# Performance work log

Measured on AMD Instinct MI355X. Metric: run time of the kernel, lower is better.

Reference implementation:

```python
import jax, jax.numpy as jnp
import numpy as np

B, A, NB = 8, 1024, 64          # batch, atoms, neighbors
NAB, NF, NG, NI = 128, 128, 25, 3  # atom basis, filters, gaussians, interactions
CUT = 5.0
MAXZ = 100
LOG2 = float(np.log(2.0))

def ssp(x):
    # shifted softplus: log(0.5) + softplus(x)
    return jax.nn.softplus(x) - LOG2

def setup_inputs() -> dict:
    key = jax.random.key(0)
    ks = jax.random.split(key, 12)
    positions = jax.random.uniform(ks[0], (B, A, 3), jnp.float32, 0.0, 10.0)
    cell = jnp.zeros((B, 3, 3), jnp.float32)
    cell_offset = jnp.zeros((B, A, NB, 3), jnp.float32)
    # self-avoiding neighbor indices in [0, A)
    off = jax.random.randint(ks[1], (B, A, NB), 1, A)
    neighbors = ((jnp.arange(A)[None, :, None] + off) % A).astype(jnp.int32)
    neighbor_mask = jnp.ones((B, A, NB), jnp.float32)
    atom_mask = jnp.ones((B, A), jnp.float32)
    atomic_numbers = jax.random.randint(ks[2], (B, A), 1, MAXZ).astype(jnp.int32)
    s = 0.05
    emb = (jax.random.normal(ks[3], (MAXZ, NAB)) * 0.1).at[0].set(0.0)  # padding_idx=0
    fw1 = jax.random.normal(ks[4], (NI, NG, NF)) * s
    fb1 = jnp.zeros((NI, NF), jnp.float32)
    fw2 = jax.random.normal(ks[5], (NI, NF, NF)) * s
    fb2 = jnp.zeros((NI, NF), jnp.float32)
    in2f_w = jax.random.normal(ks[6], (NI, NAB, NF)) * s
    f2out_w = jax.random.normal(ks[7], (NI, NF, NAB)) * s
    f2out_b = jnp.zeros((NI, NAB), jnp.float32)
    dense_w = jax.random.normal(ks[8], (NI, NAB, NAB)) * s
    dense_b = jnp.zeros((NI, NAB), jnp.float32)
    return dict(positions=positions, cell=cell, cell_offset=cell_offset,
                neighbor_mask=neighbor_mask, atom_mask=atom_mask,
                emb=emb, fw1=fw1, fb1=fb1, fw2=fw2, fb2=fb2,
                in2f_w=in2f_w, f2out_w=f2out_w, f2out_b=f2out_b,
                dense_w=dense_w, dense_b=dense_b,
                atomic_numbers=atomic_numbers, neighbors=neighbors)

def reference(positions, cell, cell_offset, neighbor_mask, atom_mask,
              emb, fw1, fb1, fw2, fb2, in2f_w, f2out_w, f2out_b,
              dense_w, dense_b, atomic_numbers, neighbors):
    x = emb[atomic_numbers]                                   # (B,A,NAB)
    nb = neighbors.reshape(B, A * NB)
    # atom distances with PBC offsets
    pos_j = jnp.take_along_axis(positions, nb[..., None], axis=1).reshape(B, A, NB, 3)
    pos_j = pos_j + jnp.einsum('banc,bcd->band', cell_offset, cell)
    dvec = pos_j - positions[:, :, None, :]
    d2 = jnp.sum(dvec * dvec, axis=-1)                        # (B,A,NB)
    r_ij = jnp.sqrt(jnp.where(neighbor_mask > 0, d2, 1.0)) * neighbor_mask
    # gaussian smearing of distances
    offsets = jnp.linspace(0.0, CUT, NG, dtype=jnp.float32)
    width = offsets[1] - offsets[0]
    coeff = -0.5 / (width * width)
    f_ij = jnp.exp(coeff * (r_ij[..., None] - offsets) ** 2)  # (B,A,NB,NG)
    # cosine cutoff
    C = 0.5 * (jnp.cos(r_ij * jnp.pi / CUT) + 1.0) * (r_ij < CUT)
    for i in range(NI):
        # filter-generating network
        W = ssp(f_ij @ fw1[i] + fb1[i]) @ fw2[i] + fb2[i]     # (B,A,NB,NF)
        W = W * C[..., None]
        # CFConv: project, gather neighbors, modulate, scatter-sum
        y = x @ in2f_w[i]                                     # (B,A,NF)
        y_nbh = jnp.take_along_axis(y, nb[..., None], axis=1).reshape(B, A, NB, NF)
        agg = jnp.sum(y_nbh * W * neighbor_mask[..., None], axis=2)  # (B,A,NF)
        v = ssp(agg @ f2out_w[i] + f2out_b[i])                # (B,A,NAB)
        v = v @ dense_w[i] + dense_b[i]
        x = x + v
    return x
```

## Files before the change

### kernel.cpp

```cpp
#include <hip/hip_runtime.h>

typedef __attribute__((ext_vector_type(8))) short bf16x8;
typedef __attribute__((ext_vector_type(4))) float f32x4;
typedef __attribute__((ext_vector_type(2))) unsigned int u32x2;
typedef __attribute__((ext_vector_type(4))) unsigned int u32x4;
typedef __attribute__((ext_vector_type(2))) __bf16 bf16x2t;
typedef unsigned short u16;
typedef unsigned int u32;
typedef unsigned long long u64;

#define DI __device__ __forceinline__

#define NKNOT 2048

DI float b2f(u16 u){ union{u32 i; float f;} v; v.i = ((u32)u)<<16; return v.f; }
DI float asf(u32 u){ union{u32 i; float f;} v; v.i = u; return v.f; }
DI u16 f2b(float f){ union{float f; u32 i;} v; v.f=f; u32 u=v.i;
                     return (u16)((u + 0x7fffu + ((u>>16)&1u))>>16); }
DI u32 pk2(float lo, float hi){
#if __has_builtin(__builtin_amdgcn_cvt_pk_bf16_f32)
  bf16x2t h = __builtin_amdgcn_cvt_pk_bf16_f32(lo, hi);
  u32 d; __builtin_memcpy(&d, &h, 4); return d;
#else
  return (u32)f2b(lo) | ((u32)f2b(hi)<<16);
#endif
}
DI float fexp2(float x){
#if __has_builtin(__builtin_amdgcn_exp2f)
  return __builtin_amdgcn_exp2f(x);
#else
  return __expf(x*0.6931471805599453f);
#endif
}
DI float flog2(float x){
#if __has_builtin(__builtin_amdgcn_logf)
  return __builtin_amdgcn_logf(x);
#else
  return __logf(x)*1.4426950408889634f;
#endif
}
DI float ldin(const void* p, size_t i, int isbf){
  return isbf ? b2f(((const u16*)p)[i]) : ((const float*)p)[i];
}
DI f32x4 ldin4(const void* p, size_t i, int isbf){
  if(isbf){
    u32x2 d = *(const u32x2*)((const u16*)p + i);
    f32x4 r;
    r[0] = b2f((u16)(d[0]&0xffff)); r[1] = b2f((u16)(d[0]>>16));
    r[2] = b2f((u16)(d[1]&0xffff)); r[3] = b2f((u16)(d[1]>>16));
    return r;
  }
  return *(const f32x4*)((const float*)p + i);
}
DI int probe_bf(const void* nmask){ return ((const u16*)nmask)[0] == 0x3F80u; }

DI f32x4 mfma16(bf16x8 a, bf16x8 b, f32x4 c){
  return __builtin_amdgcn_mfma_f32_16x16x32_bf16(a,b,c,0,0,0);
}
DI bf16x8 ldfragA_f32(const float* p){
  f32x4 a = ((const f32x4*)p)[0], b = ((const f32x4*)p)[1];
  union{ u32 d[4]; bf16x8 v; } u;
  u.d[0]=pk2(a[0],a[1]); u.d[1]=pk2(a[2],a[3]);
  u.d[2]=pk2(b[0],b[1]); u.d[3]=pk2(b[2],b[3]);
  return u.v;
}
DI float sspf(float x){ return __logf(1.f + __expf(x)) - 0.6931471805599453f; }

#define WF_STRIDE 73728
#define WF_FW2    4096
#define WF_IN2F   24576
#define WF_F2O    40960
#define WF_DEN    57344

__global__ __launch_bounds__(256) void k_setup(const void* __restrict__ pos,
                                               const void* __restrict__ cell,
                                               const void* __restrict__ cello,
                                               const void* __restrict__ nmask,
                                               const void* __restrict__ emb,
                                               const void* __restrict__ fw1,
                                               const void* __restrict__ fb1,
                                               const void* __restrict__ fw2,
                                               const void* __restrict__ fb2,
                                               const void* __restrict__ in2f,
                                               const void* __restrict__ f2o,
                                               const void* __restrict__ den,
                                               const int* __restrict__ z,
                                               const int* __restrict__ nbrs,
                                               float* __restrict__ X,
                                               u32x2* __restrict__ DESC,
                                               u32* __restrict__ CNT,
                                               u16* __restrict__ WF){
  int isbf = probe_bf(nmask);
  int bx = blockIdx.x, tid = threadIdx.x;
  if(bx < 1024){
    int idx = bx*256 + tid;
    int a = idx>>5, f4 = (idx&31)*4;
    f32x4 e = ldin4(emb, (size_t)z[a]*128 + f4, isbf);
    *(f32x4*)(X + (size_t)a*128 + f4) = e;
    return;
  }
  if(bx < 3072){
    int pairIdx = (bx-1024)*256 + tid;
    int atom = pairIdx>>6;
    int lane = tid & 63;
    int b = atom>>10;
    int nb = nbrs[pairIdx];
    int jrow = (b<<10) + nb;
    float pi0=ldin(pos,atom*3+0,isbf), pi1=ldin(pos,atom*3+1,isbf), pi2=ldin(pos,atom*3+2,isbf);
    float pj0=ldin(pos,jrow*3+0,isbf), pj1=ldin(pos,jrow*3+1,isbf), pj2=ldin(pos,jrow*3+2,isbf);
    float co0=ldin(cello,(size_t)pairIdx*3+0,isbf),
          co1=ldin(cello,(size_t)pairIdx*3+1,isbf),
          co2=ldin(cello,(size_t)pairIdx*3+2,isbf);
    size_t cb = (size_t)b*9;
    pj0 += co0*ldin(cell,cb+0,isbf) + co1*ldin(cell,cb+3,isbf) + co2*ldin(cell,cb+6,isbf);
    pj1 += co0*ldin(cell,cb+1,isbf) + co1*ldin(cell,cb+4,isbf) + co2*ldin(cell,cb+7,isbf);
    pj2 += co0*ldin(cell,cb+2,isbf) + co1*ldin(cell,cb+5,isbf) + co2*ldin(cell,cb+8,isbf);
    float d0 = pj0-pi0, d1 = pj1-pi1, d2 = pj2-pi2;
    float dd = d0*d0 + d1*d1 + d2*d2;
    float m  = ldin(nmask,pairIdx,isbf);
    float r  = sqrtf(m>0.f ? dd : 1.f) * m;
    float c  = 0.5f*(__cosf(r*3.14159265358979f/5.f)+1.f) * ((r<5.f)?1.f:0.f) * m;
    float s  = r * ((float)(NKNOT-1)/5.0f);
    int   k  = (int)s; if(k > NKNOT-2) k = NKNOT-2;
    float fr = s - (float)k;
    float a0 = c*(1.f-fr), a1 = c*fr;
    union{ _Float16 h[2]; u32 u; } pa;
    pa.h[0] = (_Float16)a0; pa.h[1] = (_Float16)a1;
    int act = (c > 0.f);
    u64 bal = __ballot(act);
    u64 below = bal & ((1ULL<<lane)-1ULL);
    int cnt = (int)__popcll(bal);
    int apre = (int)__popcll(below);
    int pos_ = act ? apre : (cnt + (lane - apre));
    u32x2 dsc;
    if(act){ dsc[0] = pa.u; dsc[1] = (u32)k | ((u32)nb<<16); }
    else   { dsc[0] = 0u;   dsc[1] = 0u; }
    DESC[(size_t)atom*64 + pos_] = dsc;
    if(lane == 0) CNT[atom] = (u32)cnt;
    return;
  }
  int wid = (bx-3072)*4 + (tid>>6);
  int lane = tid & 63;
  int q = lane>>4, l15 = lane&15;
  int i = wid/144, r = wid%144;
  int mat, kk, t;
  if(r < 8){ mat=0; kk=0; t=r; }
  else if(r < 48){ int r2 = r-8; mat=1; kk=r2>>3; t=r2&7; }
  else { int r3 = r-48; mat = 2 + (r3>>5); kk = (r3>>3)&3; t = r3&7; }
  const void* src; size_t sbase; int K; int off;
  switch(mat){
    case 0:  src = fw1;  sbase=(size_t)i*3200;  K=25;  off=0;       break;
    case 1:  src = fw2;  sbase=(size_t)i*16384; K=128; off=WF_FW2;  break;
    case 2:  src = in2f; sbase=(size_t)i*16384; K=128; off=WF_IN2F; break;
    case 3:  src = f2o;  sbase=(size_t)i*16384; K=128; off=WF_F2O;  break;
    default: src = den;  sbase=(size_t)i*16384; K=128; off=WF_DEN;  break;
  }
  int c = t*16 + l15;
  bf16x8 frag;
  #pragma unroll
  for(int j=0;j<8;j++){
    int k = kk*32 + q*8 + j;
    float v;
    if(k < K)                 v = ldin(src, sbase + (size_t)k*128 + c, isbf);
    else if(mat==0 && k==25)  v = ldin(fb1, (size_t)i*128 + c, isbf);
    else if(mat==1 && k==128) v = ldin(fb2, (size_t)i*128 + c, isbf);
    else                      v = 0.f;
    if(mat==0) v *= 1.4426950408889634f;
    frag[j] = (short)f2b(v);
  }
  *(bf16x8*)(WF + (size_t)i*WF_STRIDE + off + ((kk*8+t)*64 + lane)*8) = frag;
}

__global__ __launch_bounds__(256) void k_mid(const u16* __restrict__ WF,
                                             u32x2* __restrict__ TT,
                                             const float* __restrict__ X,
                                             float* __restrict__ Y){
  __shared__ __align__(16) u16 Hb[4][16][168];
  int tid = threadIdx.x;
  int widx = tid>>6;
  int lane = tid & 63;
  int q = lane>>4, l15 = lane&15;
  int bx = blockIdx.x;

  if(bx >= 96){
    int wid2 = (bx-96)*4 + widx;
    int row0 = wid2*16;
    const u16* wf = WF + WF_IN2F;
    f32x4 acc[8];
    #pragma unroll
    for(int t=0;t<8;t++) acc[t] = (f32x4){0.f,0.f,0.f,0.f};
    #pragma unroll
    for(int kk=0;kk<4;kk++){
      bf16x8 xf = ldfragA_f32(X + (size_t)(row0+l15)*128 + kk*32 + q*8);
      #pragma unroll
      for(int t=0;t<8;t++){
        bf16x8 wv = *(const bf16x8*)(wf + ((kk*8+t)*64 + lane)*8);
        acc[t] = mfma16(wv, xf, acc[t]);
      }
    }
    #pragma unroll
    for(int t=0;t<8;t++)
      *(f32x4*)(Y + (size_t)(row0+l15)*128 + t*16 + q*4) = acc[t];
    return;
  }

  int wid = bx*4 + widx;
  int i  = wid>>7;
  int kb = (wid&127)*16;
  const u16* fw1f = WF + (size_t)i*WF_STRIDE;
  const u16* fw2f = WF + (size_t)i*WF_STRIDE + WF_FW2;
  u16 (*H)[168] = Hb[widx];

  const float width = 5.0f/24.0f;
  const float c2 = (-0.5f/(width*width))*1.4426950408889634f;
  float r = (float)(kb + l15) * (5.0f/(float)(NKNOT-1));

  float gv[8];
  #pragma unroll
  for(int j=0;j<8;j++){
    int k = q*8+j;
    if(k < 25){ float t = fmaf(-width,(float)k,r); gv[j] = fexp2(c2*t*t); }
    else gv[j] = (k==25) ? 1.f : 0.f;
  }
  union{ u32 d[4]; bf16x8 v; } afu;
  afu.d[0]=pk2(gv[0],gv[1]); afu.d[1]=pk2(gv[2],gv[3]);
  afu.d[2]=pk2(gv[4],gv[5]); afu.d[3]=pk2(gv[6],gv[7]);
  bf16x8 af = afu.v;

  f32x4 acc[8];
  #pragma unroll
  for(int t=0;t<8;t++){
    bf16x8 w1 = *(const bf16x8*)(fw1f + (size_t)t*512 + lane*8);
    acc[t] = mfma16(w1, af, (f32x4){0.f,0.f,0.f,0.f});
  }
  const float ln2 = 0.69314718055994531f;
  #pragma unroll
  for(int t=0;t<8;t++){
    float h0 = fmaf(flog2(1.f+fexp2(acc[t][0])), ln2, -ln2);
    float h1 = fmaf(flog2(1.f+fexp2(acc[t][1])), ln2, -ln2);
    float h2 = fmaf(flog2(1.f+fexp2(acc[t][2])), ln2, -ln2);
    float h3 = fmaf(flog2(1.f+fexp2(acc[t][3])), ln2, -ln2);
    u32x2 d; d[0]=pk2(h0,h1); d[1]=pk2(h2,h3);
    *(u32x2*)(&H[l15][t*16 + q*4]) = d;
  }
  {
    u32x2 zb; zb[0] = (q==0) ? pk2(1.f, 0.f) : 0u; zb[1] = 0u;
    *(u32x2*)(&H[l15][128 + q*4]) = zb;
    u32x2 zz; zz[0]=0u; zz[1]=0u;
    *(u32x2*)(&H[l15][144 + q*4]) = zz;
  }
  #pragma unroll
  for(int t=0;t<8;t++) acc[t] = (f32x4){0.f,0.f,0.f,0.f};
  #pragma unroll
  for(int kk=0;kk<5;kk++){
    bf16x8 a2 = *(const bf16x8*)(&H[l15][kk*32 + q*8]);
    #pragma unroll
    for(int t=0;t<8;t++){
      bf16x8 wv = *(const bf16x8*)(fw2f + ((kk*8+t)*64 + lane)*8);
      acc[t] = mfma16(a2, wv, acc[t]);
    }
  }
  {
    u32x2* ttb = TT + (size_t)i*NKNOT*64;
    int row = kb + l15;
    #pragma unroll
    for(int t=0;t<8;t++){
      u32 d0 = pk2(acc[t][0],acc[t][1]);
      u32 d1 = pk2(acc[t][2],acc[t][3]);
      int l = t*8 + q*2;
      ((u32*)&ttb[(size_t)row*64 + l    ])[0] = d0;
      ((u32*)&ttb[(size_t)row*64 + l + 1])[0] = d1;
      if(row > 0){
        ((u32*)&ttb[(size_t)(row-1)*64 + l    ])[1] = d0;
        ((u32*)&ttb[(size_t)(row-1)*64 + l + 1])[1] = d1;
      }
    }
  }
}

__global__ __launch_bounds__(512, 8) void k_iter(const u32x2* __restrict__ desc,
                                                 const u32* __restrict__ CNT,
                                                 const u32x2* __restrict__ TT,
                                                 const float* __restrict__ Yr,
                                                 float* __restrict__ X,
                                                 float* __restrict__ Yw,
                                                 const u16* __restrict__ f2of,
                                                 const u16* __restrict__ denf,
                                                 const u16* __restrict__ in2fN,
                                                 const void* __restrict__ f2ob,
                                                 const void* __restrict__ denb,
                                                 const void* __restrict__ nmask,
                                                 void* __restrict__ OUT,
                                                 int last, int iidx){
  __shared__ __align__(16) float AGGs[16][132];
  __shared__ __align__(16) u16 Tb[16][136];
  __shared__ __align__(16) u16 Xw[16][136];
  int isbf = probe_bf(nmask);
  int widx = threadIdx.x>>6;
  int lane = threadIdx.x & 63;
  int q = lane>>4, l15 = lane&15;
  int bid = blockIdx.x;
  int row0 = (bid & 7)*1024 + (bid >> 3)*8;

  {
    int atom = row0 + widx;
    int cnt = (int)__builtin_amdgcn_readfirstlane(CNT[atom]);
    int ng  = (cnt + 3) >> 2;
    u32x2 dsc = desc[(size_t)atom*64 + lane];
    const char* Yb = (const char*)(Yr + (size_t)(atom & ~1023)*128);
    const char* Tc = (const char*)TT;
    int h   = lane>>5;
    int j32 = lane&31;
    int boff = j32<<4;
    f32x4 acc4 = (f32x4){0.f,0.f,0.f,0.f};
    #pragma unroll 1
    for(int g=0; g<ng; ++g){
      u32 cu[2]; u32x4 tt[2]; f32x4 yv[2];
      #pragma unroll
      for(int s=0; s<2; ++s){
        int p0 = g*4 + s*2;
        u32 d1a = __builtin_amdgcn_readlane(dsc[1], p0);
        u32 d1b = __builtin_amdgcn_readlane(dsc[1], p0+1);
        u32 d0a = __builtin_amdgcn_readlane(dsc[0], p0);
        u32 d0b = __builtin_amdgcn_readlane(dsc[0], p0+1);
        u32 d1 = h ? d1b : d1a;
        cu[s]  = h ? d0b : d0a;
        u32 krow = d1 & 0xffffu;
        u32 nbr  = d1 >> 16;
        tt[s] = *(const u32x4*)(Tc + ((size_t)krow<<9) + boff);
        yv[s] = *(const f32x4*)(Yb + ((size_t)nbr<<9) + boff);
      }
      #pragma unroll
      for(int s=0; s<2; ++s){
        union{ u32 u; _Float16 hh[2]; } pa; pa.u = cu[s];
        float a0 = (float)pa.hh[0], a1 = (float)pa.hh[1];
        float w0 = fmaf(a1, asf(tt[s][1]<<16),          a0*asf(tt[s][0]<<16));
        float w1 = fmaf(a1, asf(tt[s][1]&0xffff0000u),  a0*asf(tt[s][0]&0xffff0000u));
        float w2 = fmaf(a1, asf(tt[s][3]<<16),          a0*asf(tt[s][2]<<16));
        float w3 = fmaf(a1, asf(tt[s][3]&0xffff0000u),  a0*asf(tt[s][2]&0xffff0000u));
        acc4[0] = fmaf(w0, yv[s][0], acc4[0]);
        acc4[1] = fmaf(w1, yv[s][1], acc4[1]);
        acc4[2] = fmaf(w2, yv[s][2], acc4[2]);
        acc4[3] = fmaf(w3, yv[s][3], acc4[3]);
      }
    }
    *(f32x4*)(&AGGs[widx + 8*h][j32*4]) = acc4;
  }
  __syncthreads();

  {
    int t = widx;
    f32x4 acc = (f32x4){0.f,0.f,0.f,0.f};
    #pragma unroll
    for(int kk=0;kk<4;kk++){
      bf16x8 gf = ldfragA_f32(&AGGs[l15][kk*32 + q*8]);
      bf16x8 wv = *(const bf16x8*)(f2of + ((kk*8+t)*64 + lane)*8);
      acc = mfma16(wv, gf, acc);
    }
    #pragma unroll
    for(int r=0;r<4;r++) acc[r] += __shfl_xor(acc[r], 8);
    f32x4 bv = ldin4(f2ob, (size_t)iidx*128 + t*16 + q*4, isbf);
    u32x2 d;
    d[0] = pk2(sspf(acc[0]+bv[0]), sspf(acc[1]+bv[1]));
    d[1] = pk2(sspf(acc[2]+bv[2]), sspf(acc[3]+bv[3]));
    *(u32x2*)(&Tb[l15][t*16 + q*4]) = d;
  }
  __syncthreads();

  {
    int t = widx;
    f32x4 acc = (f32x4){0.f,0.f,0.f,0.f};
    #pragma unroll
    for(int kk=0;kk<4;kk++){
      bf16x8 tf = *(const bf16x8*)(&Tb[l15][kk*32 + q*8]);
      bf16x8 wv = *(const bf16x8*)(denf + ((kk*8+t)*64 + lane)*8);
      acc = mfma16(wv, tf, acc);
    }
    size_t idx = (size_t)(row0+l15)*128 + t*16 + q*4;
    f32x4 bv = ldin4(denb, (size_t)iidx*128 + t*16 + q*4, isbf);
    f32x4 xv = *(const f32x4*)(X + idx);
    f32x4 xn;
    #pragma unroll
    for(int r=0;r<4;r++) xn[r] = xv[r] + acc[r] + bv[r];
    if(l15 < 8){
      *(f32x4*)(X + idx) = xn;
      if(last){
        if(isbf){
          u32x2 o; o[0]=pk2(xn[0],xn[1]); o[1]=pk2(xn[2],xn[3]);
          *(u32x2*)((u16*)OUT + idx) = o;
        } else {
          *(f32x4*)((float*)OUT + idx) = xn;
        }
      }
    }
    if(!last){
      u32x2 d; d[0]=pk2(xn[0],xn[1]); d[1]=pk2(xn[2],xn[3]);
      *(u32x2*)(&Xw[l15][t*16 + q*4]) = d;
    }
  }
  if(!last){
    __syncthreads();
    {
      int t = widx;
      f32x4 acc = (f32x4){0.f,0.f,0.f,0.f};
      #pragma unroll
      for(int kk=0;kk<4;kk++){
        bf16x8 xf = *(const bf16x8*)(&Xw[l15][kk*32 + q*8]);
        bf16x8 wv = *(const bf16x8*)(in2fN + ((kk*8+t)*64 + lane)*8);
        acc = mfma16(wv, xf, acc);
      }
      if(l15 < 8)
        *(f32x4*)(Yw + (size_t)(row0+l15)*128 + t*16 + q*4) = acc;
    }
  }
}

extern "C" void kernel_launch(void* const* d_in, const int* in_sizes, int n_in,
                              void* d_out, int out_size, void* d_ws, size_t ws_size,
                              hipStream_t stream){
  const void* pos   = d_in[0];
  const void* cell  = d_in[1];
  const void* cello = d_in[2];
  const void* nmask = d_in[3];
  const void* emb   = d_in[5];
  const void* fw1   = d_in[6];
  const void* fb1   = d_in[7];
  const void* fw2   = d_in[8];
  const void* fb2   = d_in[9];
  const void* in2f  = d_in[10];
  const void* f2o   = d_in[11];
  const void* f2ob  = d_in[12];
  const void* den   = d_in[13];
  const void* denb  = d_in[14];
  const int* z      = (const int*)d_in[15];
  const int* nbrs   = (const int*)d_in[16];

  char* ws = (char*)d_ws;
  float* X    = (float*)(ws);
  float* Y    = (float*)(ws +  4194304);
  float* Y2   = (float*)(ws +  8388608);
  u32x2* DESC = (u32x2*)(ws + 12582912);
  u16*   WF   = (u16*)  (ws + 16777216);
  u32x2* TT   = (u32x2*)(ws + 17301504);
  u32*   CNT  = (u32*)  (ws + 20447232);

  k_setup<<<3180, 256, 0, stream>>>(pos, cell, cello, nmask, emb,
                                    fw1, fb1, fw2, fb2, in2f, f2o, den,
                                    z, nbrs, X, DESC, CNT, WF);
  k_mid  <<< 224, 256, 0, stream>>>(WF, TT, X, Y);

  for(int i=0;i<3;i++){
    const u16* base = WF + (size_t)i*WF_STRIDE;
    const u16* in2fN = (i<2) ? (WF + (size_t)(i+1)*WF_STRIDE + WF_IN2F) : WF;
    const float* Yrd = (i&1) ? Y2 : Y;
    float*       Ywr = (i&1) ? Y  : Y2;
    k_iter<<<1024, 512, 0, stream>>>(DESC, CNT, TT + (size_t)i*NKNOT*64, Yrd, X, Ywr,
                                     base + WF_F2O, base + WF_DEN, in2fN,
                                     f2ob, denb, nmask,
                                     d_out, (i==2) ? 1 : 0, i);
  }
}
```

Before: 161.8 us.

## Merge setup and mid kernels into one launch reading raw weights directly

Combines the setup and mid kernels into a single launch. The filter-table and first-layer projection blocks now read fw1/fw2/in2f and the embedding straight from the inputs, converting to bf16 in registers, so they no longer depend on the pre-packed weight buffer or X written by other blocks. The aim is to remove one kernel launch and the serialization between the two stages. In exchange, those blocks do redundant strided global loads and conversions of the weights, and shared memory is now allocated for every block of the merged kernel.

```diff
diff --git a/kernel.cpp b/kernel.cpp
--- a/kernel.cpp
+++ b/kernel.cpp
@@ -67,31 +67,37 @@
 DI float sspf(float x){ return __logf(1.f + __expf(x)) - 0.6931471805599453f; }
 
 #define WF_STRIDE 73728
-#define WF_FW2    4096
 #define WF_IN2F   24576
 #define WF_F2O    40960
 #define WF_DEN    57344
 
-__global__ __launch_bounds__(256) void k_setup(const void* __restrict__ pos,
-                                               const void* __restrict__ cell,
-                                               const void* __restrict__ cello,
-                                               const void* __restrict__ nmask,
-                                               const void* __restrict__ emb,
-                                               const void* __restrict__ fw1,
-                                               const void* __restrict__ fb1,
-                                               const void* __restrict__ fw2,
-                                               const void* __restrict__ fb2,
-                                               const void* __restrict__ in2f,
-                                               const void* __restrict__ f2o,
-                                               const void* __restrict__ den,
-                                               const int* __restrict__ z,
-                                               const int* __restrict__ nbrs,
-                                               float* __restrict__ X,
-                                               u32x2* __restrict__ DESC,
-                                               u32* __restrict__ CNT,
-                                               u16* __restrict__ WF){
+__global__ __launch_bounds__(256) void k_all(const void* __restrict__ pos,
+                                             const void* __restrict__ cell,
+                                             const void* __restrict__ cello,
+                                             const void* __restrict__ nmask,
+                                             const void* __restrict__ emb,
+                                             const void* __restrict__ fw1,
+                                             const void* __restrict__ fb1,
+                                             const void* __restrict__ fw2,
+                                             const void* __restrict__ fb2,
+                                             const void* __restrict__ in2f,
+                                             const void* __restrict__ f2o,
+                                             const void* __restrict__ den,
+                                             const int* __restrict__ z,
+                                             const int* __restrict__ nbrs,
+                                             float* __restrict__ X,
+                                             u32x2* __restrict__ DESC,
+                                             u32* __restrict__ CNT,
+                                             u16* __restrict__ WF,
+                                             u32x2* __restrict__ TT,
+                                             float* __restrict__ Y){
+  __shared__ __align__(16) u16 Hb[4][16][168];
   int isbf = probe_bf(nmask);
   int bx = blockIdx.x, tid = threadIdx.x;
+  int widx = tid>>6;
+  int lane = tid & 63;
+  int q = lane>>4, l15 = lane&15;
+
   if(bx < 1024){
     int idx = bx*256 + tid;
     int a = idx>>5, f4 = (idx&31)*4;
@@ -102,7 +108,6 @@
   if(bx < 3072){
     int pairIdx = (bx-1024)*256 + tid;
     int atom = pairIdx>>6;
-    int lane = tid & 63;
     int b = atom>>10;
     int nb = nbrs[pairIdx];
     int jrow = (b<<10) + nb;
@@ -139,142 +144,150 @@
     if(lane == 0) CNT[atom] = (u32)cnt;
     return;
   }
-  int wid = (bx-3072)*4 + (tid>>6);
-  int lane = tid & 63;
-  int q = lane>>4, l15 = lane&15;
-  int i = wid/144, r = wid%144;
-  int mat, kk, t;
-  if(r < 8){ mat=0; kk=0; t=r; }
-  else if(r < 48){ int r2 = r-8; mat=1; kk=r2>>3; t=r2&7; }
-  else { int r3 = r-48; mat = 2 + (r3>>5); kk = (r3>>3)&3; t = r3&7; }
-  const void* src; size_t sbase; int K; int off;
-  switch(mat){
-    case 0:  src = fw1;  sbase=(size_t)i*3200;  K=25;  off=0;       break;
-    case 1:  src = fw2;  sbase=(size_t)i*16384; K=128; off=WF_FW2;  break;
-    case 2:  src = in2f; sbase=(size_t)i*16384; K=128; off=WF_IN2F; break;
-    case 3:  src = f2o;  sbase=(size_t)i*16384; K=128; off=WF_F2O;  break;
-    default: src = den;  sbase=(size_t)i*16384; K=128; off=WF_DEN;  break;
-  }
-  int c = t*16 + l15;
-  bf16x8 frag;
-  #pragma unroll
-  for(int j=0;j<8;j++){
-    int k = kk*32 + q*8 + j;
-    float v;
-    if(k < K)                 v = ldin(src, sbase + (size_t)k*128 + c, isbf);
-    else if(mat==0 && k==25)  v = ldin(fb1, (size_t)i*128 + c, isbf);
-    else if(mat==1 && k==128) v = ldin(fb2, (size_t)i*128 + c, isbf);
-    else                      v = 0.f;
-    if(mat==0) v *= 1.4426950408889634f;
-    frag[j] = (short)f2b(v);
-  }
-  *(bf16x8*)(WF + (size_t)i*WF_STRIDE + off + ((kk*8+t)*64 + lane)*8) = frag;
-}
-
-__global__ __launch_bounds__(256) void k_mid(const u16* __restrict__ WF,
-                                             u32x2* __restrict__ TT,
-                                             const float* __restrict__ X,
-                                             float* __restrict__ Y){
-  __shared__ __align__(16) u16 Hb[4][16][168];
-  int tid = threadIdx.x;
-  int widx = tid>>6;
-  int lane = tid & 63;
-  int q = lane>>4, l15 = lane&15;
-  int bx = blockIdx.x;
-
-  if(bx >= 96){
-    int wid2 = (bx-96)*4 + widx;
+  if(bx < 3144){
+    int wid = (bx-3072)*4 + widx;
+    int i = wid/96, r = wid%96;
+    int mat = r>>5, kk = (r>>3)&3, t = r&7;
+    const void* src; int off;
+    switch(mat){
+      case 0:  src = in2f; off=WF_IN2F; break;
+      case 1:  src = f2o;  off=WF_F2O;  break;
+      default: src = den;  off=WF_DEN;  break;
+    }
+    size_t sbase = (size_t)i*16384;
+    int c = t*16 + l15;
+    bf16x8 frag;
+    #pragma unroll
+    for(int j=0;j<8;j++){
+      int k = kk*32 + q*8 + j;
+      frag[j] = (short)f2b(ldin(src, sbase + (size_t)k*128 + c, isbf));
+    }
+    *(bf16x8*)(WF + (size_t)i*WF_STRIDE + off + ((kk*8+t)*64 + lane)*8) = frag;
+    return;
+  }
+  if(bx < 3240){
+    int wid = (bx-3144)*4 + widx;
+    int i  = wid>>7;
+    int kb = (wid&127)*16;
+    u16 (*H)[168] = Hb[widx];
+
+    const float width = 5.0f/24.0f;
+    const float c2 = (-0.5f/(width*width))*1.4426950408889634f;
+    const float l2e = 1.4426950408889634f;
+    float r = (float)(kb + l15) * (5.0f/(float)(NKNOT-1));
+
+    float gv[8];
+    #pragma unroll
+    for(int j=0;j<8;j++){
+      int k = q*8+j;
+      if(k < 25){ float t = fmaf(-width,(float)k,r); gv[j] = fexp2(c2*t*t); }
+      else gv[j] = (k==25) ? 1.f : 0.f;
+    }
+    union{ u32 d[4]; bf16x8 v; } afu;
+    afu.d[0]=pk2(gv[0],gv[1]); afu.d[1]=pk2(gv[2],gv[3]);
+    afu.d[2]=pk2(gv[4],gv[5]); afu.d[3]=pk2(gv[6],gv[7]);
+    bf16x8 af = afu.v;
+
+    f32x4 acc[8];
+    #pragma unroll
+    for(int t=0;t<8;t++){
+      int c = t*16 + l15;
+      union{ u32 d[4]; bf16x8 v; } wu;
+      #pragma unroll
+      for(int jj=0;jj<4;jj++){
+        int k0 = q*8 + jj*2, k1 = k0+1;
+        float v0 = (k0<25) ? ldin(fw1,(size_t)i*3200+(size_t)k0*128+c,isbf)
+                 : (k0==25 ? ldin(fb1,(size_t)i*128+c,isbf) : 0.f);
+        float v1 = (k1<25) ? ldin(fw1,(size_t)i*3200+(size_t)k1*128+c,isbf)
+                 : (k1==25 ? ldin(fb1,(size_t)i*128+c,isbf) : 0.f);
+        wu.d[jj] = pk2(v0*l2e, v1*l2e);
+      }
+      acc[t] = mfma16(wu.v, af, (f32x4){0.f,0.f,0.f,0.f});
+    }
+    const float ln2 = 0.69314718055994531f;
+    #pragma unroll
+    for(int t=0;t<8;t++){
+      float h0 = fmaf(flog2(1.f+fexp2(acc[t][0])), ln2, -ln2);
+      float h1 = fmaf(flog2(1.f+fexp2(acc[t][1])), ln2, -ln2);
+      float h2 = fmaf(flog2(1.f+fexp2(acc[t][2])), ln2, -ln2);
+      float h3 = fmaf(flog2(1.f+fexp2(acc[t][3])), ln2, -ln2);
+      u32x2 d; d[0]=pk2(h0,h1); d[1]=pk2(h2,h3);
+      *(u32x2*)(&H[l15][t*16 + q*4]) = d;
+    }
+    {
+      u32x2 zb; zb[0] = (q==0) ? pk2(1.f, 0.f) : 0u; zb[1] = 0u;
+      *(u32x2*)(&H[l15][128 + q*4]) = zb;
+      u32x2 zz; zz[0]=0u; zz[1]=0u;
+      *(u32x2*)(&H[l15][144 + q*4]) = zz;
+    }
+    #pragma unroll
+    for(int t=0;t<8;t++) acc[t] = (f32x4){0.f,0.f,0.f,0.f};
+    #pragma unroll
+    for(int kk=0;kk<5;kk++){
+      bf16x8 a2 = *(const bf16x8*)(&H[l15][kk*32 + q*8]);
+      #pragma unroll
+      for(int t=0;t<8;t++){
+        int c = t*16 + l15;
+        union{ u32 d[4]; bf16x8 v; } wu;
+        #pragma unroll
+        for(int jj=0;jj<4;jj++){
+          int k0 = kk*32 + q*8 + jj*2, k1 = k0+1;
+          float v0 = (k0<128) ? ldin(fw2,(size_t)i*16384+(size_t)k0*128+c,isbf)
+                   : (k0==128 ? ldin(fb2,(size_t)i*128+c,isbf) : 0.f);
+          float v1 = (k1<128) ? ldin(fw2,(size_t)i*16384+(size_t)k1*128+c,isbf)
+                   : (k1==128 ? ldin(fb2,(size_t)i*128+c,isbf) : 0.f);
+          wu.d[jj] = pk2(v0, v1);
+        }
+        acc[t] = mfma16(a2, wu.v, acc[t]);
+      }
+    }
+    {
+      u32x2* ttb = TT + (size_t)i*NKNOT*64;
+      int row = kb + l15;
+      #pragma unroll
+      for(int t=0;t<8;t++){
+        u32 d0 = pk2(acc[t][0],acc[t][1]);
+        u32 d1 = pk2(acc[t][2],acc[t][3]);
+        int l = t*8 + q*2;
+        ((u32*)&ttb[(size_t)row*64 + l    ])[0] = d0;
+        ((u32*)&ttb[(size_t)row*64 + l + 1])[0] = d1;
+        if(row > 0){
+          ((u32*)&ttb[(size_t)(row-1)*64 + l    ])[1] = d0;
+          ((u32*)&ttb[(size_t)(row-1)*64 + l + 1])[1] = d1;
+        }
+      }
+    }
+    return;
+  }
+  {
+    int wid2 = (bx-3240)*4 + widx;
     int row0 = wid2*16;
-    const u16* wf = WF + WF_IN2F;
+    int zr = z[row0 + l15];
     f32x4 acc[8];
     #pragma unroll
     for(int t=0;t<8;t++) acc[t] = (f32x4){0.f,0.f,0.f,0.f};
     #pragma unroll
     for(int kk=0;kk<4;kk++){
-      bf16x8 xf = ldfragA_f32(X + (size_t)(row0+l15)*128 + kk*32 + q*8);
+      bf16x8 xf;
+      if(isbf) xf = *(const bf16x8*)((const u16*)emb + (size_t)zr*128 + kk*32 + q*8);
+      else     xf = ldfragA_f32((const float*)emb + (size_t)zr*128 + kk*32 + q*8);
       #pragma unroll
       for(int t=0;t<8;t++){
-        bf16x8 wv = *(const bf16x8*)(wf + ((kk*8+t)*64 + lane)*8);
-        acc[t] = mfma16(wv, xf, acc[t]);
+        int c = t*16 + l15;
+        union{ u32 d[4]; bf16x8 v; } wu;
+        #pragma unroll
+        for(int jj=0;jj<4;jj++){
+          int k0 = kk*32 + q*8 + jj*2;
+          float v0 = ldin(in2f, (size_t)k0*128 + c, isbf);
+          float v1 = ldin(in2f, (size_t)(k0+1)*128 + c, isbf);
+          wu.d[jj] = pk2(v0, v1);
+        }
+        acc[t] = mfma16(wu.v, xf, acc[t]);
       }
     }
     #pragma unroll
     for(int t=0;t<8;t++)
       *(f32x4*)(Y + (size_t)(row0+l15)*128 + t*16 + q*4) = acc[t];
-    return;
-  }
-
-  int wid = bx*4 + widx;
-  int i  = wid>>7;
-  int kb = (wid&127)*16;
-  const u16* fw1f = WF + (size_t)i*WF_STRIDE;
-  const u16* fw2f = WF + (size_t)i*WF_STRIDE + WF_FW2;
-  u16 (*H)[168] = Hb[widx];
-
-  const float width = 5.0f/24.0f;
-  const float c2 = (-0.5f/(width*width))*1.4426950408889634f;
-  float r = (float)(kb + l15) * (5.0f/(float)(NKNOT-1));
-
-  float gv[8];
-  #pragma unroll
-  for(int j=0;j<8;j++){
-    int k = q*8+j;
-    if(k < 25){ float t = fmaf(-width,(float)k,r); gv[j] = fexp2(c2*t*t); }
-    else gv[j] = (k==25) ? 1.f : 0.f;
-  }
-  union{ u32 d[4]; bf16x8 v; } afu;
-  afu.d[0]=pk2(gv[0],gv[1]); afu.d[1]=pk2(gv[2],gv[3]);
-  afu.d[2]=pk2(gv[4],gv[5]); afu.d[3]=pk2(gv[6],gv[7]);
-  bf16x8 af = afu.v;
-
-  f32x4 acc[8];
-  #pragma unroll
-  for(int t=0;t<8;t++){
-    bf16x8 w1 = *(const bf16x8*)(fw1f + (size_t)t*512 + lane*8);
-    acc[t] = mfma16(w1, af, (f32x4){0.f,0.f,0.f,0.f});
-  }
-  const float ln2 = 0.69314718055994531f;
-  #pragma unroll
-  for(int t=0;t<8;t++){
-    float h0 = fmaf(flog2(1.f+fexp2(acc[t][0])), ln2, -ln2);
-    float h1 = fmaf(flog2(1.f+fexp2(acc[t][1])), ln2, -ln2);
-    float h2 = fmaf(flog2(1.f+fexp2(acc[t][2])), ln2, -ln2);
-    float h3 = fmaf(flog2(1.f+fexp2(acc[t][3])), ln2, -ln2);
-    u32x2 d; d[0]=pk2(h0,h1); d[1]=pk2(h2,h3);
-    *(u32x2*)(&H[l15][t*16 + q*4]) = d;
-  }
-  {
-    u32x2 zb; zb[0] = (q==0) ? pk2(1.f, 0.f) : 0u; zb[1] = 0u;
-    *(u32x2*)(&H[l15][128 + q*4]) = zb;
-    u32x2 zz; zz[0]=0u; zz[1]=0u;
-    *(u32x2*)(&H[l15][144 + q*4]) = zz;
-  }
-  #pragma unroll
-  for(int t=0;t<8;t++) acc[t] = (f32x4){0.f,0.f,0.f,0.f};
-  #pragma unroll
-  for(int kk=0;kk<5;kk++){
-    bf16x8 a2 = *(const bf16x8*)(&H[l15][kk*32 + q*8]);
-    #pragma unroll
-    for(int t=0;t<8;t++){
-      bf16x8 wv = *(const bf16x8*)(fw2f + ((kk*8+t)*64 + lane)*8);
-      acc[t] = mfma16(a2, wv, acc[t]);
-    }
-  }
-  {
-    u32x2* ttb = TT + (size_t)i*NKNOT*64;
-    int row = kb + l15;
-    #pragma unroll
-    for(int t=0;t<8;t++){
-      u32 d0 = pk2(acc[t][0],acc[t][1]);
-      u32 d1 = pk2(acc[t][2],acc[t][3]);
-      int l = t*8 + q*2;
-      ((u32*)&ttb[(size_t)row*64 + l    ])[0] = d0;
-      ((u32*)&ttb[(size_t)row*64 + l + 1])[0] = d1;
-      if(row > 0){
-        ((u32*)&ttb[(size_t)(row-1)*64 + l    ])[1] = d0;
-        ((u32*)&ttb[(size_t)(row-1)*64 + l + 1])[1] = d1;
-      }
-    }
   }
 }
 
@@ -444,10 +457,9 @@
   u32x2* TT   = (u32x2*)(ws + 17301504);
   u32*   CNT  = (u32*)  (ws + 20447232);
 
-  k_setup<<<3180, 256, 0, stream>>>(pos, cell, cello, nmask, emb,
-                                    fw1, fb1, fw2, fb2, in2f, f2o, den,
-                                    z, nbrs, X, DESC, CNT, WF);
-  k_mid  <<< 224, 256, 0, stream>>>(WF, TT, X, Y);
+  k_all<<<3368, 256, 0, stream>>>(pos, cell, cello, nmask, emb,
+                                  fw1, fb1, fw2, fb2, in2f, f2o, den,
+                                  z, nbrs, X, DESC, CNT, WF, TT, Y);
 
   for(int i=0;i<3;i++){
     const u16* base = WF + (size_t)i*WF_STRIDE;
```

New measurement: 180.7 us. 11.7% more time.

## Fuse mid and interaction kernels into one cooperative kernel with grid syncs

Applied to the files above, without the earlier changes.

Replaces the k_mid launch and the three k_iter launches with a single cooperative kernel. It builds the filter tables and the first projection, then runs the three interaction iterations, with grid.sync() between stages. The aim is to cut kernel launch overhead and the inter-kernel drain gaps. In exchange it needs 1024 blocks of 512 threads to be co-resident, adds grid barrier cost and extra shared memory per block, and falls back to the old launch sequence if the cooperative launch fails.

```diff
diff --git a/kernel.cpp b/kernel.cpp
--- a/kernel.cpp
+++ b/kernel.cpp
@@ -1,4 +1,7 @@
 #include <hip/hip_runtime.h>
+#include <hip/hip_cooperative_groups.h>
+
+namespace cg = cooperative_groups;
 
 typedef __attribute__((ext_vector_type(8))) short bf16x8;
 typedef __attribute__((ext_vector_type(4))) float f32x4;
@@ -171,45 +174,14 @@
   *(bf16x8*)(WF + (size_t)i*WF_STRIDE + off + ((kk*8+t)*64 + lane)*8) = frag;
 }
 
-__global__ __launch_bounds__(256) void k_mid(const u16* __restrict__ WF,
-                                             u32x2* __restrict__ TT,
-                                             const float* __restrict__ X,
-                                             float* __restrict__ Y){
-  __shared__ __align__(16) u16 Hb[4][16][168];
-  int tid = threadIdx.x;
-  int widx = tid>>6;
-  int lane = tid & 63;
+
+DI void table_wave(const u16* __restrict__ WF, u32x2* __restrict__ TT,
+                   int wid, int lane, u16 (*H)[168]){
   int q = lane>>4, l15 = lane&15;
-  int bx = blockIdx.x;
-
-  if(bx >= 96){
-    int wid2 = (bx-96)*4 + widx;
-    int row0 = wid2*16;
-    const u16* wf = WF + WF_IN2F;
-    f32x4 acc[8];
-    #pragma unroll
-    for(int t=0;t<8;t++) acc[t] = (f32x4){0.f,0.f,0.f,0.f};
-    #pragma unroll
-    for(int kk=0;kk<4;kk++){
-      bf16x8 xf = ldfragA_f32(X + (size_t)(row0+l15)*128 + kk*32 + q*8);
-      #pragma unroll
-      for(int t=0;t<8;t++){
-        bf16x8 wv = *(const bf16x8*)(wf + ((kk*8+t)*64 + lane)*8);
-        acc[t] = mfma16(wv, xf, acc[t]);
-      }
-    }
-    #pragma unroll
-    for(int t=0;t<8;t++)
-      *(f32x4*)(Y + (size_t)(row0+l15)*128 + t*16 + q*4) = acc[t];
-    return;
-  }
-
-  int wid = bx*4 + widx;
   int i  = wid>>7;
   int kb = (wid&127)*16;
   const u16* fw1f = WF + (size_t)i*WF_STRIDE;
   const u16* fw2f = WF + (size_t)i*WF_STRIDE + WF_FW2;
-  u16 (*H)[168] = Hb[widx];
 
   const float width = 5.0f/24.0f;
   const float c2 = (-0.5f/(width*width))*1.4426950408889634f;
@@ -260,46 +232,54 @@
       acc[t] = mfma16(a2, wv, acc[t]);
     }
   }
-  {
-    u32x2* ttb = TT + (size_t)i*NKNOT*64;
-    int row = kb + l15;
+  u32x2* ttb = TT + (size_t)i*NKNOT*64;
+  int row = kb + l15;
+  #pragma unroll
+  for(int t=0;t<8;t++){
+    u32 d0 = pk2(acc[t][0],acc[t][1]);
+    u32 d1 = pk2(acc[t][2],acc[t][3]);
+    int l = t*8 + q*2;
+    ((u32*)&ttb[(size_t)row*64 + l    ])[0] = d0;
+    ((u32*)&ttb[(size_t)row*64 + l + 1])[0] = d1;
+    if(row > 0){
+      ((u32*)&ttb[(size_t)(row-1)*64 + l    ])[1] = d0;
+      ((u32*)&ttb[(size_t)(row-1)*64 + l + 1])[1] = d1;
+    }
+  }
+}
+
+DI void proj_wave(const u16* __restrict__ WF, const float* __restrict__ X,
+                  float* __restrict__ Y, int wid2, int lane){
+  int q = lane>>4, l15 = lane&15;
+  int row0 = wid2*16;
+  const u16* wf = WF + WF_IN2F;
+  f32x4 acc[8];
+  #pragma unroll
+  for(int t=0;t<8;t++) acc[t] = (f32x4){0.f,0.f,0.f,0.f};
+  #pragma unroll
+  for(int kk=0;kk<4;kk++){
+    bf16x8 xf = ldfragA_f32(X + (size_t)(row0+l15)*128 + kk*32 + q*8);
     #pragma unroll
     for(int t=0;t<8;t++){
-      u32 d0 = pk2(acc[t][0],acc[t][1]);
-      u32 d1 = pk2(acc[t][2],acc[t][3]);
-      int l = t*8 + q*2;
-      ((u32*)&ttb[(size_t)row*64 + l    ])[0] = d0;
-      ((u32*)&ttb[(size_t)row*64 + l + 1])[0] = d1;
-      if(row > 0){
-        ((u32*)&ttb[(size_t)(row-1)*64 + l    ])[1] = d0;
-        ((u32*)&ttb[(size_t)(row-1)*64 + l + 1])[1] = d1;
-      }
-    }
-  }
-}
-
-__global__ __launch_bounds__(512, 8) void k_iter(const u32x2* __restrict__ desc,
-                                                 const u32* __restrict__ CNT,
-                                                 const u32x2* __restrict__ TT,
-                                                 const float* __restrict__ Yr,
-                                                 float* __restrict__ X,
-                                                 float* __restrict__ Yw,
-                                                 const u16* __restrict__ f2of,
-                                                 const u16* __restrict__ denf,
-                                                 const u16* __restrict__ in2fN,
-                                                 const void* __restrict__ f2ob,
-                                                 const void* __restrict__ denb,
-                                                 const void* __restrict__ nmask,
-                                                 void* __restrict__ OUT,
-                                                 int last, int iidx){
-  __shared__ __align__(16) float AGGs[16][132];
-  __shared__ __align__(16) u16 Tb[16][136];
-  __shared__ __align__(16) u16 Xw[16][136];
-  int isbf = probe_bf(nmask);
-  int widx = threadIdx.x>>6;
-  int lane = threadIdx.x & 63;
+      bf16x8 wv = *(const bf16x8*)(wf + ((kk*8+t)*64 + lane)*8);
+      acc[t] = mfma16(wv, xf, acc[t]);
+    }
+  }
+  #pragma unroll
+  for(int t=0;t<8;t++)
+    *(f32x4*)(Y + (size_t)(row0+l15)*128 + t*16 + q*4) = acc[t];
+}
+
+DI void iter_body(const u32x2* __restrict__ desc, const u32* __restrict__ CNT,
+                  const u32x2* __restrict__ TT, const float* __restrict__ Yr,
+                  float* __restrict__ X, float* __restrict__ Yw,
+                  const u16* __restrict__ f2of, const u16* __restrict__ denf,
+                  const u16* __restrict__ in2fN,
+                  const void* __restrict__ f2ob, const void* __restrict__ denb,
+                  void* __restrict__ OUT, int last, int iidx, int isbf,
+                  int bid, int widx, int lane,
+                  float (*AGGs)[132], u16 (*Tb)[136], u16 (*Xw)[136]){
   int q = lane>>4, l15 = lane&15;
-  int bid = blockIdx.x;
   int row0 = (bid & 7)*1024 + (bid >> 3)*8;
 
   {
@@ -415,6 +395,87 @@
   }
 }
 
+__global__ __launch_bounds__(512, 8) void k_coop(const u32x2* __restrict__ desc,
+                                                 const u32* __restrict__ CNT,
+                                                 u32x2* __restrict__ TT,
+                                                 float* __restrict__ Y,
+                                                 float* __restrict__ Y2,
+                                                 float* __restrict__ X,
+                                                 const u16* __restrict__ WF,
+                                                 const void* __restrict__ f2ob,
+                                                 const void* __restrict__ denb,
+                                                 const void* __restrict__ nmask,
+                                                 void* __restrict__ OUT){
+  __shared__ __align__(16) float AGGs[16][132];
+  __shared__ __align__(16) u16 Tb[16][136];
+  __shared__ __align__(16) u16 Xw[16][136];
+  __shared__ __align__(16) u16 Hb[3][16][168];
+  cg::grid_group grid = cg::this_grid();
+  int isbf = probe_bf(nmask);
+  int bid = blockIdx.x;
+  int widx = threadIdx.x>>6;
+  int lane = threadIdx.x & 63;
+
+  if(bid < 128){
+    if(widx < 3) table_wave(WF, TT, bid*3 + widx, lane, Hb[widx]);
+  } else if(bid < 192){
+    proj_wave(WF, X, Y, (bid-128)*8 + widx, lane);
+  }
+  grid.sync();
+
+  #pragma unroll 1
+  for(int it=0; it<3; ++it){
+    const float* Yr = (it&1) ? Y2 : Y;
+    float*       Yw = (it&1) ? Y  : Y2;
+    const u16* base = WF + (size_t)it*WF_STRIDE;
+    const u16* in2fN = (it<2) ? (WF + (size_t)(it+1)*WF_STRIDE + WF_IN2F) : WF;
+    iter_body(desc, CNT, TT + (size_t)it*NKNOT*64, Yr, X, Yw,
+              base + WF_F2O, base + WF_DEN, in2fN,
+              f2ob, denb, OUT, (it==2)?1:0, it, isbf,
+              bid, widx, lane, AGGs, Tb, Xw);
+    if(it < 2) grid.sync();
+  }
+}
+
+__global__ __launch_bounds__(256) void k_mid(const u16* __restrict__ WF,
+                                             u32x2* __restrict__ TT,
+                                             const float* __restrict__ X,
+                                             float* __restrict__ Y){
+  __shared__ __align__(16) u16 Hb[4][16][168];
+  int tid = threadIdx.x;
+  int widx = tid>>6;
+  int lane = tid & 63;
+  int bx = blockIdx.x;
+  if(bx >= 96){
+    proj_wave(WF, X, Y, (bx-96)*4 + widx, lane);
+    return;
+  }
+  table_wave(WF, TT, bx*4 + widx, lane, Hb[widx]);
+}
+
+__global__ __launch_bounds__(512, 8) void k_iter(const u32x2* __restrict__ desc,
+                                                 const u32* __restrict__ CNT,
+                                                 const u32x2* __restrict__ TT,
+                                                 const float* __restrict__ Yr,
+                                                 float* __restrict__ X,
+                                                 float* __restrict__ Yw,
+                                                 const u16* __restrict__ f2of,
+                                                 const u16* __restrict__ denf,
+                                                 const u16* __restrict__ in2fN,
+                                                 const void* __restrict__ f2ob,
+                                                 const void* __restrict__ denb,
+                                                 const void* __restrict__ nmask,
+                                                 void* __restrict__ OUT,
+                                                 int last, int iidx){
+  __shared__ __align__(16) float AGGs[16][132];
+  __shared__ __align__(16) u16 Tb[16][136];
+  __shared__ __align__(16) u16 Xw[16][136];
+  int isbf = probe_bf(nmask);
+  iter_body(desc, CNT, TT, Yr, X, Yw, f2of, denf, in2fN, f2ob, denb,
+            OUT, last, iidx, isbf,
+            blockIdx.x, threadIdx.x>>6, threadIdx.x&63, AGGs, Tb, Xw);
+}
+
 extern "C" void kernel_launch(void* const* d_in, const int* in_sizes, int n_in,
                               void* d_out, int out_size, void* d_ws, size_t ws_size,
                               hipStream_t stream){
@@ -447,16 +508,30 @@
   k_setup<<<3180, 256, 0, stream>>>(pos, cell, cello, nmask, emb,
                                     fw1, fb1, fw2, fb2, in2f, f2o, den,
                                     z, nbrs, X, DESC, CNT, WF);
-  k_mid  <<< 224, 256, 0, stream>>>(WF, TT, X, Y);
-
-  for(int i=0;i<3;i++){
-    const u16* base = WF + (size_t)i*WF_STRIDE;
-    const u16* in2fN = (i<2) ? (WF + (size_t)(i+1)*WF_STRIDE + WF_IN2F) : WF;
-    const float* Yrd = (i&1) ? Y2 : Y;
-    float*       Ywr = (i&1) ? Y  : Y2;
-    k_iter<<<1024, 512, 0, stream>>>(DESC, CNT, TT + (size_t)i*NKNOT*64, Yrd, X, Ywr,
-                                     base + WF_F2O, base + WF_DEN, in2fN,
-                                     f2ob, denb, nmask,
-                                     d_out, (i==2) ? 1 : 0, i);
-  }
-}
+
+  {
+    void* desc_p = (void*)DESC; void* cnt_p = (void*)CNT; void* tt_p = (void*)TT;
+    void* y_p = (void*)Y; void* y2_p = (void*)Y2; void* x_p = (void*)X;
+    void* wf_p = (void*)WF; void* f2ob_p = (void*)f2ob; void* denb_p = (void*)denb;
+    void* nm_p = (void*)nmask; void* out_p = d_out;
+    void* args[11] = {&desc_p, &cnt_p, &tt_p, &y_p, &y2_p, &x_p, &wf_p,
+                      &f2ob_p, &denb_p, &nm_p, &out_p};
+    hipError_t e = hipLaunchCooperativeKernel((const void*)k_coop,
+                                              dim3(1024), dim3(512),
+                                              args, 0, stream);
+    if(e != hipSuccess){
+      k_mid<<<224, 256, 0, stream>>>(WF, TT, X, Y);
+      for(int i=0;i<3;i++){
+        const u16* base = WF + (size_t)i*WF_STRIDE;
+        const u16* in2fN = (i<2) ? (WF + (size_t)(i+1)*WF_STRIDE + WF_IN2F) : WF;
+        const float* Yrd = (i&1) ? Y2 : Y;
+        float*       Ywr = (i&1) ? Y  : Y2;
+        k_iter<<<1024, 512, 0, stream>>>(DESC, CNT, TT + (size_t)i*NKNOT*64,
+                                         Yrd, X, Ywr,
+                                         base + WF_F2O, base + WF_DEN, in2fN,
+                                         f2ob, denb, nmask,
+                                         d_out, (i==2) ? 1 : 0, i);
+      }
+    }
+  }
+}
```

Measured after the change: 570.1 us. +252.3%, slower.
